# Optimization experiments

Measured on AMD Instinct MI355X. Metric: run time of the kernel, lower is better.

Reference implementation:

```python
import jax, jax.numpy as jnp
import numpy as np


def setup_inputs() -> dict:
    key = jax.random.key(0)
    k1, k2, k3 = jax.random.split(key, 3)
    B, S, D_IN, D_OUT = 4, 2048, 4096, 4096
    x = jax.random.normal(k1, (B, S, D_IN), dtype=jnp.float32)
    weight = jax.random.normal(k2, (D_OUT, D_IN), dtype=jnp.float32) * 0.02
    bias = jax.random.normal(k3, (D_OUT,), dtype=jnp.float32) * 0.02
    return {"x": x, "weight": weight, "bias": bias}


def reference(x, weight, bias):
    # Column L1 norms over the output dim (torch.norm(w, p=1, dim=0)) -> [in_features]
    column_norms = jnp.abs(weight).sum(axis=0)
    q = jnp.quantile(column_norms, jnp.array([0.05, 0.95], dtype=column_norms.dtype))
    lower, upper = q[0], q[1]
    # NOTE: mask naming follows the source; 'outlier_columns' is actually the middle band.
    outlier_columns = (column_norms > lower) & (column_norms < upper)  # [in]
    binarized = ~outlier_columns  # columns that get rescaled (mask is inverted in source)

    # Row-wise abs-mean over the 'binarized' columns, detached. Shape [out, 1].
    n_bin = binarized.sum().astype(weight.dtype)
    scale = (jnp.abs(weight) * binarized[None, :]).sum(axis=-1, keepdims=True) / n_bin
    scale = jax.lax.stop_gradient(scale)

    # The STE sign assignment in the source is overwritten by w * scale, so the
    # effective binarized-column value is weight * scale (not sign(weight) * scale).
    w_bin = jnp.where(binarized[None, :], weight * scale, weight)  # [out, in]

    # F.linear(x, w_bin, bias)
    out = jnp.einsum('bsd,od->bso', x, w_bin) + bias
    return out
```

## Files before the change

### kernel.cpp

```cpp
#include <hip/hip_runtime.h>
#include <hip/hip_bf16.h>

typedef unsigned short u16;
typedef __bf16 bf16x8 __attribute__((ext_vector_type(8)));
typedef float f32x4 __attribute__((ext_vector_type(4)));
typedef __attribute__((address_space(1))) void* gp1_t;
typedef __attribute__((address_space(3))) void* lp3_t;

#define D_IN   4096
#define D_OUT  4096
#define M_ROWS 8192

#define OFF_NORMS  0u
#define OFF_QVALS  16384u
#define OFF_XB     573696u
#define OFF_WB     67682560u

static __device__ __forceinline__ u16 f2bf(float f) {
    __hip_bfloat16 h = __float2bfloat16(f);
    u16 u; __builtin_memcpy(&u, &h, 2);
    return u;
}

__global__ __launch_bounds__(256) void k1_cast_colnorm(const float* __restrict__ x,
                                                       const float* __restrict__ W,
                                                       u16* __restrict__ xb,
                                                       float* __restrict__ norms) {
    const int b = blockIdx.x;
    if (b < 512) {
        const int j  = (b & 15) * 256 + threadIdx.x;
        const int r0 = (b >> 4) * 128;
        float s = 0.f;
        #pragma unroll 4
        for (int r = 0; r < 128; ++r) s += fabsf(W[(size_t)(r0 + r) * D_IN + j]);
        atomicAdd(&norms[j], s);
    } else {
        const size_t i4 = (size_t)(b - 512) * 256 + threadIdx.x;
        const float4 v = ((const float4*)x)[i4];
        ushort4 r;
        r.x = f2bf(v.x); r.y = f2bf(v.y); r.z = f2bf(v.z); r.w = f2bf(v.w);
        ((ushort4*)xb)[i4] = r;
    }
}

__global__ void rank_select(const float* __restrict__ norms, float* __restrict__ qvals) {
    __shared__ float sn[D_IN];
    const int tid = threadIdx.x;
    for (int i = tid; i < D_IN; i += 256) sn[i] = norms[i];
    __syncthreads();
    const int j = blockIdx.x * 256 + tid;
    const float vj = sn[j];
    int r = 0;
    #pragma unroll 8
    for (int i = 0; i < D_IN; ++i) {
        const float vi = sn[i];
        r += (vi < vj) || (vi == vj && i < j);
    }
    if      (r == 204)  qvals[0] = vj;
    else if (r == 205)  qvals[1] = vj;
    else if (r == 3890) qvals[2] = vj;
    else if (r == 3891) qvals[3] = vj;
}

__global__ __launch_bounds__(256) void k3_scale_wbin(const float* __restrict__ W,
                                                     const float* __restrict__ norms,
                                                     const float* __restrict__ qvals,
                                                     u16* __restrict__ wb) {
    __shared__ float red[8];
    const int o = blockIdx.x, t = threadIdx.x;
    const int wave = t >> 6, lane = t & 63;
    const float lower = qvals[0] + 0.75f * (qvals[1] - qvals[0]);
    const float upper = qvals[2] + 0.25f * (qvals[3] - qvals[2]);
    const float4* row4 = (const float4*)(W + (size_t)o * D_IN);
    const float4* n4   = (const float4*)norms;

    float4 wv[4];
    int binbits[4];
    float cnt = 0.f, sum = 0.f;
    #pragma unroll
    for (int it = 0; it < 4; ++it) {
        const int c = it * 256 + t;
        wv[it] = row4[c];
        const float4 nv = n4[c];
        const bool b0 = !(nv.x > lower && nv.x < upper);
        const bool b1 = !(nv.y > lower && nv.y < upper);
        const bool b2 = !(nv.z > lower && nv.z < upper);
        const bool b3 = !(nv.w > lower && nv.w < upper);
        binbits[it] = (b0 ? 1 : 0) | (b1 ? 2 : 0) | (b2 ? 4 : 0) | (b3 ? 8 : 0);
        cnt += (float)(b0 + b1 + b2 + b3);
        sum += (b0 ? fabsf(wv[it].x) : 0.f) + (b1 ? fabsf(wv[it].y) : 0.f)
             + (b2 ? fabsf(wv[it].z) : 0.f) + (b3 ? fabsf(wv[it].w) : 0.f);
    }
    #pragma unroll
    for (int off = 32; off > 0; off >>= 1) {
        cnt += __shfl_down(cnt, off, 64);
        sum += __shfl_down(sum, off, 64);
    }
    if (lane == 0) { red[wave] = cnt; red[4 + wave] = sum; }
    __syncthreads();
    const float nbin = red[0] + red[1] + red[2] + red[3];
    const float ssum = red[4] + red[5] + red[6] + red[7];
    const float sc = ssum / nbin;

    ushort4* out = (ushort4*)(wb + (size_t)o * D_IN);
    #pragma unroll
    for (int it = 0; it < 4; ++it) {
        const int c = it * 256 + t;
        const int bb = binbits[it];
        ushort4 r;
        r.x = f2bf((bb & 1) ? wv[it].x * sc : wv[it].x);
        r.y = f2bf((bb & 2) ? wv[it].y * sc : wv[it].y);
        r.z = f2bf((bb & 4) ? wv[it].z * sc : wv[it].z);
        r.w = f2bf((bb & 8) ? wv[it].w * sc : wv[it].w);
        out[c] = r;
    }
}

__global__ __launch_bounds__(256) void gemm_bt(const u16* __restrict__ A, const u16* __restrict__ B,
                                               const float* __restrict__ bias, float* __restrict__ C) {
    __shared__ u16 lA[128 * 32];
    __shared__ u16 lB[128 * 32];
    const int tid  = threadIdx.x;
    const int wave = tid >> 6, lane = tid & 63;
    const int wr = wave >> 1, wc = wave & 1;
    const int m0 = blockIdx.y * 128, n0 = blockIdx.x * 128;

    const int r    = tid >> 2;
    const int cc   = ((tid & 3) - ((r >> 1) & 3)) & 3;
    const int scol = cc * 8;
    const u16* gA0 = A + (size_t)(m0 + r) * D_IN + scol;
    const u16* gA1 = A + (size_t)(m0 + 64 + r) * D_IN + scol;
    const u16* gB0 = B + (size_t)(n0 + r) * D_IN + scol;
    const u16* gB1 = B + (size_t)(n0 + 64 + r) * D_IN + scol;
    lp3_t lA0 = (lp3_t)(lA + wave * 512);
    lp3_t lA1 = (lp3_t)(lA + 2048 + wave * 512);
    lp3_t lB0 = (lp3_t)(lB + wave * 512);
    lp3_t lB1 = (lp3_t)(lB + 2048 + wave * 512);

    f32x4 acc[4][4] = {};

    const int cl   = lane >> 4;
    const int rsel = lane & 15;

    for (int kt = 0; kt < D_IN; kt += 32) {
        __builtin_amdgcn_global_load_lds((gp1_t)(gA0 + kt), lA0, 16, 0, 0);
        __builtin_amdgcn_global_load_lds((gp1_t)(gA1 + kt), lA1, 16, 0, 0);
        __builtin_amdgcn_global_load_lds((gp1_t)(gB0 + kt), lB0, 16, 0, 0);
        __builtin_amdgcn_global_load_lds((gp1_t)(gB1 + kt), lB1, 16, 0, 0);
        __syncthreads();

        bf16x8 af[4], bfv[4];
        #pragma unroll
        for (int mi = 0; mi < 4; ++mi) {
            const int row = wr * 64 + mi * 16 + rsel;
            const int s = row * 4 + ((cl + (row >> 1)) & 3);
            af[mi] = *(const bf16x8*)(lA + s * 8);
        }
        #pragma unroll
        for (int ni = 0; ni < 4; ++ni) {
            const int row = wc * 64 + ni * 16 + rsel;
            const int s = row * 4 + ((cl + (row >> 1)) & 3);
            bfv[ni] = *(const bf16x8*)(lB + s * 8);
        }
        #pragma unroll
        for (int mi = 0; mi < 4; ++mi)
            #pragma unroll
            for (int ni = 0; ni < 4; ++ni)
                acc[mi][ni] = __builtin_amdgcn_mfma_f32_16x16x32_bf16(af[mi], bfv[ni], acc[mi][ni], 0, 0, 0);
        __syncthreads();
    }

    const int cm = (lane >> 4) * 4;
    const int cn = lane & 15;
    #pragma unroll
    for (int ni = 0; ni < 4; ++ni) {
        const int n = n0 + wc * 64 + ni * 16 + cn;
        const float bv = bias[n];
        #pragma unroll
        for (int mi = 0; mi < 4; ++mi) {
            const int mbase = m0 + wr * 64 + mi * 16 + cm;
            #pragma unroll
            for (int rr = 0; rr < 4; ++rr)
                C[(size_t)(mbase + rr) * D_OUT + n] = acc[mi][ni][rr] + bv;
        }
    }
}

extern "C" void kernel_launch(void* const* d_in, const int* in_sizes, int n_in,
                              void* d_out, int out_size, void* d_ws, size_t ws_size,
                              hipStream_t stream) {
    const float* x    = (const float*)d_in[0];
    const float* W    = (const float*)d_in[1];
    const float* bias = (const float*)d_in[2];
    float* out = (float*)d_out;

    char* ws = (char*)d_ws;
    float* norms = (float*)(ws + OFF_NORMS);
    float* qvals = (float*)(ws + OFF_QVALS);
    u16*   xb    = (u16*)(ws + OFF_XB);
    u16*   wb    = (u16*)(ws + OFF_WB);

    hipMemsetAsync(norms, 0, D_IN * sizeof(float), stream);
    k1_cast_colnorm<<<512 + 32768, 256, 0, stream>>>(x, W, xb, norms);
    rank_select<<<16, 256, 0, stream>>>(norms, qvals);
    k3_scale_wbin<<<4096, 256, 0, stream>>>(W, norms, qvals, wb);
    gemm_bt<<<dim3(D_OUT / 128, M_ROWS / 128), 256, 0, stream>>>(xb, wb, bias, out);
}
```

Baseline: 675.4 us.

## Rewrite GEMM as 256x256 double-buffered 8-wave pipelined MFMA kernel

Replaces the 128x128 single-buffered GEMM with a 256x256-tile kernel using 8 waves, double-buffered LDS split into K halves, and an unrolled phase schedule that overlaps global->LDS loads with MFMA work. It adds an XOR-swizzled LDS layout, a block-index swizzle for L2 locality, explicit waitcnt/barrier control and setprio around MFMA bursts. The goal is to hide load latency and raise data reuse per tile. The cost is heavy use of LDS (128KB) and registers, and fragile hand-tuned synchronization.

```diff
diff --git a/kernel.cpp b/kernel.cpp
--- a/kernel.cpp
+++ b/kernel.cpp
@@ -116,74 +116,132 @@
     }
 }
 
-__global__ __launch_bounds__(256) void gemm_bt(const u16* __restrict__ A, const u16* __restrict__ B,
-                                               const float* __restrict__ bias, float* __restrict__ C) {
-    __shared__ u16 lA[128 * 32];
-    __shared__ u16 lB[128 * 32];
+
+#define BAR() do { asm volatile("" ::: "memory"); __builtin_amdgcn_s_barrier(); \
+                   asm volatile("" ::: "memory"); } while (0)
+
+#define LDA(buf, kh, mf) \
+    (*(const bf16x8*)(smA + (buf)*32768 + (kh)*16384 + wr*8192 + (mf)*1024 + lane_rd))
+#define LDB(buf, kh, nf) \
+    (*(const bf16x8*)(smB + (buf)*32768 + (kh)*16384 + wc*4096 + (nf)*1024 + lane_rd))
+
+#define STAGE_A(buf, kh, t) do { \
+    char* l_ = smA + (buf)*32768 + (kh)*16384 + wofs; \
+    __builtin_amdgcn_global_load_lds((gp1_t)(srcA0 + (t)*128 + (kh)*64), (lp3_t)l_, 16, 0, 0); \
+    __builtin_amdgcn_global_load_lds((gp1_t)(srcA1 + (t)*128 + (kh)*64), (lp3_t)(l_ + 8192), 16, 0, 0); \
+} while (0)
+
+#define STAGE_B(buf, kh, t) do { \
+    char* l_ = smB + (buf)*32768 + (kh)*16384 + wofs; \
+    __builtin_amdgcn_global_load_lds((gp1_t)(srcB0 + (t)*128 + (kh)*64), (lp3_t)l_, 16, 0, 0); \
+    __builtin_amdgcn_global_load_lds((gp1_t)(srcB1 + (t)*128 + (kh)*64), (lp3_t)(l_ + 8192), 16, 0, 0); \
+} while (0)
+
+#define MFMA __builtin_amdgcn_mfma_f32_16x16x32_bf16
+
+#define PHASE(buf, kh, mg, RB, ST, VM) do { \
+    bf16x8 a0_, a1_, a2_, a3_; \
+    if (RB) { \
+        bfr0 = LDB(buf, kh, 0); bfr1 = LDB(buf, kh, 1); \
+        bfr2 = LDB(buf, kh, 2); bfr3 = LDB(buf, kh, 3); \
+    } \
+    a0_ = LDA(buf, kh, (mg)*4 + 0); \
+    a1_ = LDA(buf, kh, (mg)*4 + 1); \
+    a2_ = LDA(buf, kh, (mg)*4 + 2); \
+    a3_ = LDA(buf, kh, (mg)*4 + 3); \
+    ST; \
+    if (VM) { asm volatile("s_waitcnt vmcnt(4)" ::: "memory"); } \
+    BAR(); \
+    asm volatile("s_waitcnt lgkmcnt(0)" ::: "memory"); \
+    __builtin_amdgcn_sched_barrier(0); \
+    __builtin_amdgcn_s_setprio(1); \
+    acc[(mg)*4+0][0] = MFMA(a0_, bfr0, acc[(mg)*4+0][0], 0, 0, 0); \
+    acc[(mg)*4+0][1] = MFMA(a0_, bfr1, acc[(mg)*4+0][1], 0, 0, 0); \
+    acc[(mg)*4+0][2] = MFMA(a0_, bfr2, acc[(mg)*4+0][2], 0, 0, 0); \
+    acc[(mg)*4+0][3] = MFMA(a0_, bfr3, acc[(mg)*4+0][3], 0, 0, 0); \
+    acc[(mg)*4+1][0] = MFMA(a1_, bfr0, acc[(mg)*4+1][0], 0, 0, 0); \
+    acc[(mg)*4+1][1] = MFMA(a1_, bfr1, acc[(mg)*4+1][1], 0, 0, 0); \
+    acc[(mg)*4+1][2] = MFMA(a1_, bfr2, acc[(mg)*4+1][2], 0, 0, 0); \
+    acc[(mg)*4+1][3] = MFMA(a1_, bfr3, acc[(mg)*4+1][3], 0, 0, 0); \
+    acc[(mg)*4+2][0] = MFMA(a2_, bfr0, acc[(mg)*4+2][0], 0, 0, 0); \
+    acc[(mg)*4+2][1] = MFMA(a2_, bfr1, acc[(mg)*4+2][1], 0, 0, 0); \
+    acc[(mg)*4+2][2] = MFMA(a2_, bfr2, acc[(mg)*4+2][2], 0, 0, 0); \
+    acc[(mg)*4+2][3] = MFMA(a2_, bfr3, acc[(mg)*4+2][3], 0, 0, 0); \
+    acc[(mg)*4+3][0] = MFMA(a3_, bfr0, acc[(mg)*4+3][0], 0, 0, 0); \
+    acc[(mg)*4+3][1] = MFMA(a3_, bfr1, acc[(mg)*4+3][1], 0, 0, 0); \
+    acc[(mg)*4+3][2] = MFMA(a3_, bfr2, acc[(mg)*4+3][2], 0, 0, 0); \
+    acc[(mg)*4+3][3] = MFMA(a3_, bfr3, acc[(mg)*4+3][3], 0, 0, 0); \
+    __builtin_amdgcn_s_setprio(0); \
+    BAR(); \
+} while (0)
+
+__global__ __launch_bounds__(512, 2) void gemm8(const u16* __restrict__ A, const u16* __restrict__ B,
+                                                const float* __restrict__ bias, float* __restrict__ C) {
+    __shared__ u16 sA[2][2][256 * 32];
+    __shared__ u16 sB[2][2][256 * 32];
+    char* const smA = (char*)&sA[0][0][0];
+    char* const smB = (char*)&sB[0][0][0];
+
     const int tid  = threadIdx.x;
     const int wave = tid >> 6, lane = tid & 63;
-    const int wr = wave >> 1, wc = wave & 1;
-    const int m0 = blockIdx.y * 128, n0 = blockIdx.x * 128;
-
-    const int r    = tid >> 2;
-    const int cc   = ((tid & 3) - ((r >> 1) & 3)) & 3;
-    const int scol = cc * 8;
-    const u16* gA0 = A + (size_t)(m0 + r) * D_IN + scol;
-    const u16* gA1 = A + (size_t)(m0 + 64 + r) * D_IN + scol;
-    const u16* gB0 = B + (size_t)(n0 + r) * D_IN + scol;
-    const u16* gB1 = B + (size_t)(n0 + 64 + r) * D_IN + scol;
-    lp3_t lA0 = (lp3_t)(lA + wave * 512);
-    lp3_t lA1 = (lp3_t)(lA + 2048 + wave * 512);
-    lp3_t lB0 = (lp3_t)(lB + wave * 512);
-    lp3_t lB1 = (lp3_t)(lB + 2048 + wave * 512);
-
-    f32x4 acc[4][4] = {};
-
-    const int cl   = lane >> 4;
-    const int rsel = lane & 15;
-
-    for (int kt = 0; kt < D_IN; kt += 32) {
-        __builtin_amdgcn_global_load_lds((gp1_t)(gA0 + kt), lA0, 16, 0, 0);
-        __builtin_amdgcn_global_load_lds((gp1_t)(gA1 + kt), lA1, 16, 0, 0);
-        __builtin_amdgcn_global_load_lds((gp1_t)(gB0 + kt), lB0, 16, 0, 0);
-        __builtin_amdgcn_global_load_lds((gp1_t)(gB1 + kt), lB1, 16, 0, 0);
-        __syncthreads();
-
-        bf16x8 af[4], bfv[4];
-        #pragma unroll
-        for (int mi = 0; mi < 4; ++mi) {
-            const int row = wr * 64 + mi * 16 + rsel;
-            const int s = row * 4 + ((cl + (row >> 1)) & 3);
-            af[mi] = *(const bf16x8*)(lA + s * 8);
-        }
-        #pragma unroll
-        for (int ni = 0; ni < 4; ++ni) {
-            const int row = wc * 64 + ni * 16 + rsel;
-            const int s = row * 4 + ((cl + (row >> 1)) & 3);
-            bfv[ni] = *(const bf16x8*)(lB + s * 8);
-        }
-        #pragma unroll
-        for (int mi = 0; mi < 4; ++mi)
-            #pragma unroll
-            for (int ni = 0; ni < 4; ++ni)
-                acc[mi][ni] = __builtin_amdgcn_mfma_f32_16x16x32_bf16(af[mi], bfv[ni], acc[mi][ni], 0, 0, 0);
-        __syncthreads();
-    }
-
-    const int cm = (lane >> 4) * 4;
-    const int cn = lane & 15;
-    #pragma unroll
-    for (int ni = 0; ni < 4; ++ni) {
-        const int n = n0 + wc * 64 + ni * 16 + cn;
+    const int wr = wave >> 2, wc = wave & 3;
+    const int r15 = lane & 15, q = lane >> 4;
+    const int wofs = wave * 1024;
+
+    const int swz = ((int)blockIdx.x & 7) * 64 + ((int)blockIdx.x >> 3);
+    const int by = swz >> 4, bx = swz & 15;
+    const int m0 = by * 256, n0 = bx * 256;
+
+    const int lane_rd = (r15 * 64 + q * 16) ^ (((r15 >> 1) & 7) << 4);
+
+    const int P0  = wofs + lane * 16;
+    const int xv  = ((lane >> 3) & 7) << 4;
+    const int lb0 = P0 ^ xv;
+    const int lb1 = (P0 + 8192) ^ xv;
+    const char* const gA = (const char*)(A + (size_t)m0 * D_IN);
+    const char* const gB = (const char*)(B + (size_t)n0 * D_IN);
+    const char* const srcA0 = gA + (size_t)(lb0 >> 6) * (D_IN * 2) + (lb0 & 63);
+    const char* const srcA1 = gA + (size_t)(lb1 >> 6) * (D_IN * 2) + (lb1 & 63);
+    const char* const srcB0 = gB + (size_t)(lb0 >> 6) * (D_IN * 2) + (lb0 & 63);
+    const char* const srcB1 = gB + (size_t)(lb1 >> 6) * (D_IN * 2) + (lb1 & 63);
+
+    f32x4 acc[8][4] = {};
+    bf16x8 bfr0{}, bfr1{}, bfr2{}, bfr3{};
+
+    STAGE_A(0, 0, 0); STAGE_B(0, 0, 0);
+    STAGE_A(0, 1, 0); STAGE_B(0, 1, 0);
+    STAGE_A(1, 0, 1); STAGE_B(1, 0, 1);
+    asm volatile("s_waitcnt vmcnt(4)" ::: "memory");
+    BAR();
+
+    for (int i = 0; i < 32; ++i) {
+        const int t1 = 2 * i + 1;
+        const int t2 = (2 * i + 2 > 63) ? 63 : 2 * i + 2;
+        const int t3 = (2 * i + 3 > 63) ? 63 : 2 * i + 3;
+        PHASE(0, 0, 0, 1, STAGE_A(1, 1, t1), 0);
+        PHASE(0, 0, 1, 0, STAGE_B(1, 1, t1), 0);
+        PHASE(0, 1, 0, 1, STAGE_A(0, 0, t2), 0);
+        PHASE(0, 1, 1, 0, STAGE_B(0, 0, t2), 1);
+        PHASE(1, 0, 0, 1, STAGE_A(0, 1, t2), 0);
+        PHASE(1, 0, 1, 0, STAGE_B(0, 1, t2), 0);
+        PHASE(1, 1, 0, 1, STAGE_A(1, 0, t3), 0);
+        PHASE(1, 1, 1, 0, STAGE_B(1, 0, t3), 1);
+    }
+
+    const int cm = q * 4;
+    #pragma unroll
+    for (int nf = 0; nf < 4; ++nf) {
+        const int n = n0 + wc * 64 + nf * 16 + r15;
         const float bv = bias[n];
         #pragma unroll
-        for (int mi = 0; mi < 4; ++mi) {
-            const int mbase = m0 + wr * 64 + mi * 16 + cm;
+        for (int mf = 0; mf < 8; ++mf) {
+            const int mbase = m0 + wr * 128 + mf * 16 + cm;
             #pragma unroll
             for (int rr = 0; rr < 4; ++rr)
-                C[(size_t)(mbase + rr) * D_OUT + n] = acc[mi][ni][rr] + bv;
+                C[(size_t)(mbase + rr) * D_OUT + n] = acc[mf][nf][rr] + bv;
         }
     }
+    asm volatile("s_waitcnt vmcnt(0)" ::: "memory");
 }
 
 extern "C" void kernel_launch(void* const* d_in, const int* in_sizes, int n_in,
@@ -204,5 +262,5 @@
     k1_cast_colnorm<<<512 + 32768, 256, 0, stream>>>(x, W, xb, norms);
     rank_select<<<16, 256, 0, stream>>>(norms, qvals);
     k3_scale_wbin<<<4096, 256, 0, stream>>>(W, norms, qvals, wb);
-    gemm_bt<<<dim3(D_OUT / 128, M_ROWS / 128), 256, 0, stream>>>(xb, wb, bias, out);
-}
+    gemm8<<<dim3(512), dim3(512), 0, stream>>>(xb, wb, bias, out);
+}
```

Result: faster. 647.9 us (-4.1%).
